# Optimization experiments

Hardware: AMD Instinct MI355X
Metric: run time of the kernel (lower is better)

Reference implementation:

```python
import jax, jax.numpy as jnp
import numpy as np

INIT_W = 0.1  # init_weight uniform range


def setup_inputs() -> dict:
    key = jax.random.key(0)
    kq, kk, kwq, kwk, ka = jax.random.split(key, 5)
    B, b, t_q, t_k = 2, 16, 64, 128
    qs = ks = nu = 512
    query = jax.random.normal(kq, (B, b, t_q, qs), dtype=jnp.float32)
    keys = jax.random.normal(kk, (B, b, t_k, ks), dtype=jnp.float32)
    # torch Linear weight layout: (out_features, in_features), per fusion slice
    Wq = (jax.random.uniform(kwq, (B, nu, qs), dtype=jnp.float32) * 2 - 1) * INIT_W
    Wk = (jax.random.uniform(kwk, (B, nu, ks), dtype=jnp.float32) * 2 - 1) * INIT_W
    linear_att = (jax.random.uniform(ka, (nu,), dtype=jnp.float32) * 2 - 1) * INIT_W
    return {"query": query, "keys": keys, "Wq": Wq, "Wk": Wk, "linear_att": linear_att}


def reference(query, keys, Wq, Wk, linear_att):
    # query: (B, b, t_q, query_size), keys: (B, b, t_k, key_size)
    # HFTA-fused linear projections (no bias): y = x @ W.T per fusion slice
    pq = jnp.einsum('Bbqi,Boi->Bbqo', query, Wq)   # (B, b, t_q, n)
    pk = jnp.einsum('Bbki,Boi->Bbko', keys, Wk)    # (B, b, t_k, n)
    # Bahdanau additive score: tanh(q + k) . v  (broadcast add over t_q x t_k)
    sum_qk = pq[:, :, :, None, :] + pk[:, :, None, :, :]   # (B, b, t_q, t_k, n)
    scores = jnp.einsum('Bbqkn,n->Bbqk', jnp.tanh(sum_qk), linear_att)
    scores_normalized = jax.nn.softmax(scores, axis=-1)    # (B, b, t_q, t_k)
    # context uses RAW keys (not projected)
    context = jnp.einsum('Bbqk,Bbkn->Bbqn', scores_normalized, keys)
    return context, scores_normalized
```

## Files before the change

### kernel.cpp

```cpp
#include <hip/hip_runtime.h>


#define DEV_INLINE __device__ __forceinline__

constexpr float C2    = 2.8853900817779268f;
constexpr float LOG2E = 1.4426950408889634f;

typedef _Float16 f16x8 __attribute__((ext_vector_type(8)));
typedef float    f32x16 __attribute__((ext_vector_type(16)));

DEV_INLINE unsigned int pk2(float a, float b) {
    auto h = __builtin_amdgcn_cvt_pkrtz(a, b);
    return __builtin_bit_cast(unsigned int, h);
}

#define GL2LDS16(g, l) __builtin_amdgcn_global_load_lds( \
    (const __attribute__((address_space(1))) void*)(g),  \
    (__attribute__((address_space(3))) void*)(l), 16, 0, 0)

__global__ __launch_bounds__(256)
void cvt_f16_kernel(const float* __restrict__ query, const float* __restrict__ keys,
                    const float* __restrict__ Wq,    const float* __restrict__ Wk,
                    uint2* __restrict__ dst)
{
    const int i4 = blockIdx.x * 256 + threadIdx.x;
    const float* src; int base;
    if (i4 < 262144)      { src = query; base = 0; }
    else if (i4 < 786432) { src = keys;  base = 262144; }
    else if (i4 < 917504) { src = Wq;    base = 786432; }
    else                  { src = Wk;    base = 917504; }
    const float4 v = *reinterpret_cast<const float4*>(src + (size_t)(i4 - base) * 4);
    dst[i4] = make_uint2(pk2(v.x, v.y), pk2(v.z, v.w));
}

__global__ __launch_bounds__(256)
void proj_mfma_kernel(const _Float16* __restrict__ X16,
                      float* __restrict__ pqT, float* __restrict__ pkT)
{
    __shared__ __align__(16) unsigned char smem[24576];

    const int bid = (blockIdx.x & 7) * 48 + (blockIdx.x >> 3);

    int Bi, mt, tt, tkshift;
    const _Float16 *Wb, *Xb; float* Y;
    if (bid < 128) {
        Bi = bid >> 6; mt = (bid >> 4) & 3; tt = bid & 15;
        Xb = X16 + ((size_t)Bi * 1024 + tt * 64) * 512;
        Wb = X16 + 3145728 + (size_t)Bi * 262144 + (size_t)(mt * 128) * 512;
        Y = pqT; tkshift = 6;
    } else {
        const int b2 = bid - 128;
        Bi = b2 >> 7; mt = (b2 >> 5) & 3; tt = b2 & 31;
        Xb = X16 + 1048576 + ((size_t)Bi * 2048 + tt * 64) * 512;
        Wb = X16 + 3670016 + (size_t)Bi * 262144 + (size_t)(mt * 128) * 512;
        Y = pkT; tkshift = 7;
    }
    const int tid = threadIdx.x;

    auto srcoff = [](int u) {
        const int row = u >> 2, s = (u & 3) ^ ((row >> 1) & 3);
        return (size_t)row * 512 + s * 8;
    };
    const _Float16* gA0 = Wb + srcoff(tid);
    const _Float16* gA1 = Wb + srcoff(tid + 256);
    const _Float16* gB  = Xb + srcoff(tid);
    unsigned char* const ldsA0 = smem + tid * 16;
    unsigned char* const ldsA1 = smem + 4096 + tid * 16;
    unsigned char* const ldsB  = smem + 8192 + tid * 16;

    const int wid = tid >> 6, lane = tid & 63;
    const int wm = wid >> 1, wn = wid & 1;
    const int r31 = lane & 31, h = lane >> 5;
    auto lofs = [](int row, int slot) {
        return row * 64 + ((slot ^ ((row >> 1) & 3)) * 16);
    };
    const int rowA0 = wm * 64 + r31, rowA1 = rowA0 + 32, rowB = wn * 32 + r31;
    const int a00 = lofs(rowA0, h),     a01 = lofs(rowA0, 2 + h);
    const int a10 = lofs(rowA1, h),     a11 = lofs(rowA1, 2 + h);
    const int b0  = 8192 + lofs(rowB, h), b1 = 8192 + lofs(rowB, 2 + h);

    f32x16 acc0, acc1;
#pragma unroll
    for (int i = 0; i < 16; ++i) { acc0[i] = 0.f; acc1[i] = 0.f; }

    GL2LDS16(gA0, ldsA0);
    GL2LDS16(gA1, ldsA1);
    GL2LDS16(gB,  ldsB);
    asm volatile("s_waitcnt vmcnt(0)" ::: "memory");
    __builtin_amdgcn_s_barrier();

    for (int ks = 0; ks < 16; ++ks) {
        const int buf = ks & 1;
        if (ks < 15) {
            const int ko = (ks + 1) * 32, bo = (buf ^ 1) * 12288;
            GL2LDS16(gA0 + ko, ldsA0 + bo);
            GL2LDS16(gA1 + ko, ldsA1 + bo);
            GL2LDS16(gB  + ko, ldsB  + bo);
        }
        const unsigned char* sb = smem + buf * 12288;
        const f16x8 fa00 = *reinterpret_cast<const f16x8*>(sb + a00);
        const f16x8 fa01 = *reinterpret_cast<const f16x8*>(sb + a01);
        const f16x8 fa10 = *reinterpret_cast<const f16x8*>(sb + a10);
        const f16x8 fa11 = *reinterpret_cast<const f16x8*>(sb + a11);
        const f16x8 fb0  = *reinterpret_cast<const f16x8*>(sb + b0);
        const f16x8 fb1  = *reinterpret_cast<const f16x8*>(sb + b1);
        acc0 = __builtin_amdgcn_mfma_f32_32x32x16_f16(fa00, fb0, acc0, 0, 0, 0);
        acc0 = __builtin_amdgcn_mfma_f32_32x32x16_f16(fa01, fb1, acc0, 0, 0, 0);
        acc1 = __builtin_amdgcn_mfma_f32_32x32x16_f16(fa10, fb0, acc1, 0, 0, 0);
        acc1 = __builtin_amdgcn_mfma_f32_32x32x16_f16(fa11, fb1, acc1, 0, 0, 0);
        if (ks < 15) {
            asm volatile("s_waitcnt vmcnt(0)" ::: "memory");
            __builtin_amdgcn_s_barrier();
        }
    }

    const int TK = 1 << tkshift;
    const int trow = tt * 64 + wn * 32 + r31;
    const int slice = Bi * 16 + (trow >> tkshift);
    const int t = trow & (TK - 1);
    const int nf0 = mt * 128 + wm * 64 + 4 * h;
#pragma unroll
    for (int ab = 0; ab < 2; ++ab) {
        const f32x16 acc = ab ? acc1 : acc0;
#pragma unroll
        for (int reg = 0; reg < 16; ++reg) {
            const int nf = nf0 + ab * 32 + (reg & 3) + 8 * (reg >> 2);
            Y[((size_t)(slice * 512 + nf) << tkshift) + t] = acc[reg] * C2;
        }
    }
}

DEV_INLINE float wave_rmax(float v) {
#pragma unroll
    for (int off = 32; off; off >>= 1) v = fmaxf(v, __shfl_xor(v, off, 64));
    return v;
}
DEV_INLINE float wave_rsum(float v) {
#pragma unroll
    for (int off = 32; off; off >>= 1) v += __shfl_xor(v, off, 64);
    return v;
}

__global__ __launch_bounds__(1024)
void score_ctx_kernel(const float* __restrict__ pqT,
                      const float* __restrict__ pkT,
                      const float* __restrict__ vatt,
                      const float* __restrict__ keys,
                      float* __restrict__ sc_out,
                      float* __restrict__ ctx)
{
    const int xcd = blockIdx.x & 7, ix = blockIdx.x >> 3;
    const int slice = xcd * 4 + (ix >> 4);
    const int q0    = (ix & 15) * 4;
    const int tid   = threadIdx.x;
    const int k     = tid & 127;
    const int nh    = tid >> 7;

    __shared__ __align__(16) float pql[512][4];
    __shared__ float wl[512];
    __shared__ float partial[7][4][128];
    __shared__ __align__(16) float sc[4][128];
    __shared__ __align__(16) float4 ctxp[4][128];
    __shared__ float wredm[8], wreds[8], wsum[8];

    if (tid < 512) {
        const float vv = vatt[tid];
        wl[tid] = -2.f * vv;
        const float4 q4 = *reinterpret_cast<const float4*>(
            pqT + ((size_t)slice * 512 + tid) * 64 + q0);
        *reinterpret_cast<float4*>(&pql[tid][0]) = q4;
        const float s = wave_rsum(vv);
        if ((tid & 63) == 0) wsum[tid >> 6] = s;
    }
    __syncthreads();
    float sumv = 0.f;
#pragma unroll
    for (int w = 0; w < 8; ++w) sumv += wsum[w];

    const float* __restrict__ pkp = pkT + ((size_t)slice * 512 + nh * 64) * 128 + k;
    float a0 = 0.f, a1 = 0.f, a2 = 0.f, a3 = 0.f;
#pragma unroll 4
    for (int n = 0; n < 64; ++n) {
        const float pk = pkp[(size_t)n * 128];
        const float4 pq4 = *reinterpret_cast<const float4*>(&pql[nh * 64 + n][0]);
        const float w = wl[nh * 64 + n];
        const float e0 = __builtin_amdgcn_exp2f(pq4.x + pk);
        const float e1 = __builtin_amdgcn_exp2f(pq4.y + pk);
        const float e2 = __builtin_amdgcn_exp2f(pq4.z + pk);
        const float e3 = __builtin_amdgcn_exp2f(pq4.w + pk);
        a0 = fmaf(w, __builtin_amdgcn_rcpf(e0 + 1.f), a0);
        a1 = fmaf(w, __builtin_amdgcn_rcpf(e1 + 1.f), a1);
        a2 = fmaf(w, __builtin_amdgcn_rcpf(e2 + 1.f), a2);
        a3 = fmaf(w, __builtin_amdgcn_rcpf(e3 + 1.f), a3);
    }
    if (nh) {
        partial[nh - 1][0][k] = a0; partial[nh - 1][1][k] = a1;
        partial[nh - 1][2][k] = a2; partial[nh - 1][3][k] = a3;
    }
    __syncthreads();
    if (!nh) {
        float s0 = a0 + sumv, s1 = a1 + sumv, s2 = a2 + sumv, s3 = a3 + sumv;
#pragma unroll
        for (int p = 0; p < 7; ++p) {
            s0 += partial[p][0][k]; s1 += partial[p][1][k];
            s2 += partial[p][2][k]; s3 += partial[p][3][k];
        }
        sc[0][k] = s0; sc[1][k] = s1; sc[2][k] = s2; sc[3][k] = s3;
    }
    __syncthreads();

    {
        const int j = nh & 3;
        float e = 0.f;
        if (tid < 512) {
            const float orig = sc[j][k];
            const float m0 = wave_rmax(orig);
            if ((tid & 63) == 0) wredm[tid >> 6] = m0;
            e = orig;
        }
        __syncthreads();
        if (tid < 512) {
            const float m = fmaxf(wredm[2 * j], wredm[2 * j + 1]);
            e = __builtin_amdgcn_exp2f((e - m) * LOG2E);
            const float ss = wave_rsum(e);
            if ((tid & 63) == 0) wreds[tid >> 6] = ss;
        }
        __syncthreads();
        if (tid < 512) {
            const float s = wreds[2 * j] + wreds[2 * j + 1];
            const float p = e * __builtin_amdgcn_rcpf(s);
            sc_out[((size_t)slice * 64 + q0 + j) * 128 + k] = p;
            sc[j][k] = p;
        }
    }
    __syncthreads();

    const int q = tid >> 8, n4 = k, ks = (tid >> 7) & 1;
    const float* __restrict__ kb = keys + (size_t)slice * 65536 + (size_t)ks * 64 * 512 + n4 * 4;
    float4 acc = {0.f, 0.f, 0.f, 0.f};
#pragma unroll 2
    for (int k4 = 0; k4 < 16; ++k4) {
        const float4 pv = *reinterpret_cast<const float4*>(&sc[q][ks * 64 + k4 * 4]);
        const float4 kv0 = *reinterpret_cast<const float4*>(kb + (size_t)(k4 * 4 + 0) * 512);
        const float4 kv1 = *reinterpret_cast<const float4*>(kb + (size_t)(k4 * 4 + 1) * 512);
        const float4 kv2 = *reinterpret_cast<const float4*>(kb + (size_t)(k4 * 4 + 2) * 512);
        const float4 kv3 = *reinterpret_cast<const float4*>(kb + (size_t)(k4 * 4 + 3) * 512);
        acc.x = fmaf(pv.x, kv0.x, acc.x); acc.y = fmaf(pv.x, kv0.y, acc.y);
        acc.z = fmaf(pv.x, kv0.z, acc.z); acc.w = fmaf(pv.x, kv0.w, acc.w);
        acc.x = fmaf(pv.y, kv1.x, acc.x); acc.y = fmaf(pv.y, kv1.y, acc.y);
        acc.z = fmaf(pv.y, kv1.z, acc.z); acc.w = fmaf(pv.y, kv1.w, acc.w);
        acc.x = fmaf(pv.z, kv2.x, acc.x); acc.y = fmaf(pv.z, kv2.y, acc.y);
        acc.z = fmaf(pv.z, kv2.z, acc.z); acc.w = fmaf(pv.z, kv2.w, acc.w);
        acc.x = fmaf(pv.w, kv3.x, acc.x); acc.y = fmaf(pv.w, kv3.y, acc.y);
        acc.z = fmaf(pv.w, kv3.z, acc.z); acc.w = fmaf(pv.w, kv3.w, acc.w);
    }
    if (ks) ctxp[q][n4] = acc;
    __syncthreads();
    if (!ks) {
        const float4 o = ctxp[q][n4];
        acc.x += o.x; acc.y += o.y; acc.z += o.z; acc.w += o.w;
        *reinterpret_cast<float4*>(ctx + ((size_t)slice * 64 + q0 + q) * 512 + n4 * 4) = acc;
    }
}

extern "C" void kernel_launch(void* const* d_in, const int* in_sizes, int n_in,
                              void* d_out, int out_size, void* d_ws, size_t ws_size,
                              hipStream_t stream)
{
    const float* query = (const float*)d_in[0];
    const float* keys  = (const float*)d_in[1];
    const float* Wq    = (const float*)d_in[2];
    const float* Wk    = (const float*)d_in[3];
    const float* vatt  = (const float*)d_in[4];

    float* ctx_out = (float*)d_out;
    float* sc_out  = ctx_out + (size_t)32 * 64 * 512;

    float* pqT = (float*)d_ws;
    float* pkT = pqT + (size_t)32 * 512 * 64;
    _Float16* X16 = (_Float16*)((char*)d_ws + 12 * 1024 * 1024);

    cvt_f16_kernel<<<dim3(4096), 256, 0, stream>>>(query, keys, Wq, Wk, (uint2*)X16);
    proj_mfma_kernel<<<dim3(384), 256, 0, stream>>>(X16, pqT, pkT);
    score_ctx_kernel<<<dim3(512), 1024, 0, stream>>>(pqT, pkT, vatt, keys, sc_out, ctx_out);
}
```

Measured before the change: 65.34 us.

## Reuse key loads across four queries in context GEMV and use bit-trick reciprocal

The context stage is restructured so each thread loads a key row once and applies it to all four queries, with the score buffer transposed to [k][q] for float4 reads. The reduction over eight key groups becomes a three-level shared-memory tree, which adds barriers. The score loop's hardware reciprocal is replaced by a bit-trick initial guess refined by two Newton iterations, presumably to move work off the transcendental unit at the cost of extra ALU ops and slightly different accuracy.

```diff
diff --git a/kernel.cpp b/kernel.cpp
--- a/kernel.cpp
+++ b/kernel.cpp
@@ -12,6 +12,13 @@
 DEV_INLINE unsigned int pk2(float a, float b) {
     auto h = __builtin_amdgcn_cvt_pkrtz(a, b);
     return __builtin_bit_cast(unsigned int, h);
+}
+
+DEV_INLINE float rcp_nr(float d) {
+    float y = __builtin_bit_cast(float, 0x7EF311C3u - __builtin_bit_cast(unsigned int, d));
+    y = y * (2.0f - d * y);
+    y = y * (2.0f - d * y);
+    return y;
 }
 
 #define GL2LDS16(g, l) __builtin_amdgcn_global_load_lds( \
@@ -159,8 +166,8 @@
     __shared__ __align__(16) float pql[512][4];
     __shared__ float wl[512];
     __shared__ float partial[7][4][128];
-    __shared__ __align__(16) float sc[4][128];
-    __shared__ __align__(16) float4 ctxp[4][128];
+    __shared__ __align__(16) float sc[128][4];
+    __shared__ __align__(16) float4 ctxp[4][4][128];
     __shared__ float wredm[8], wreds[8], wsum[8];
 
     if (tid < 512) {
@@ -188,10 +195,10 @@
         const float e1 = __builtin_amdgcn_exp2f(pq4.y + pk);
         const float e2 = __builtin_amdgcn_exp2f(pq4.z + pk);
         const float e3 = __builtin_amdgcn_exp2f(pq4.w + pk);
-        a0 = fmaf(w, __builtin_amdgcn_rcpf(e0 + 1.f), a0);
-        a1 = fmaf(w, __builtin_amdgcn_rcpf(e1 + 1.f), a1);
-        a2 = fmaf(w, __builtin_amdgcn_rcpf(e2 + 1.f), a2);
-        a3 = fmaf(w, __builtin_amdgcn_rcpf(e3 + 1.f), a3);
+        a0 = fmaf(w, rcp_nr(e0 + 1.f), a0);
+        a1 = fmaf(w, rcp_nr(e1 + 1.f), a1);
+        a2 = fmaf(w, rcp_nr(e2 + 1.f), a2);
+        a3 = fmaf(w, rcp_nr(e3 + 1.f), a3);
     }
     if (nh) {
         partial[nh - 1][0][k] = a0; partial[nh - 1][1][k] = a1;
@@ -205,7 +212,8 @@
             s0 += partial[p][0][k]; s1 += partial[p][1][k];
             s2 += partial[p][2][k]; s3 += partial[p][3][k];
         }
-        sc[0][k] = s0; sc[1][k] = s1; sc[2][k] = s2; sc[3][k] = s3;
+        float4 sv; sv.x = s0; sv.y = s1; sv.z = s2; sv.w = s3;
+        *reinterpret_cast<float4*>(&sc[k][0]) = sv;
     }
     __syncthreads();
 
@@ -213,7 +221,7 @@
         const int j = nh & 3;
         float e = 0.f;
         if (tid < 512) {
-            const float orig = sc[j][k];
+            const float orig = sc[k][j];
             const float m0 = wave_rmax(orig);
             if ((tid & 63) == 0) wredm[tid >> 6] = m0;
             e = orig;
@@ -230,36 +238,73 @@
             const float s = wreds[2 * j] + wreds[2 * j + 1];
             const float p = e * __builtin_amdgcn_rcpf(s);
             sc_out[((size_t)slice * 64 + q0 + j) * 128 + k] = p;
-            sc[j][k] = p;
-        }
-    }
-    __syncthreads();
-
-    const int q = tid >> 8, n4 = k, ks = (tid >> 7) & 1;
-    const float* __restrict__ kb = keys + (size_t)slice * 65536 + (size_t)ks * 64 * 512 + n4 * 4;
-    float4 acc = {0.f, 0.f, 0.f, 0.f};
-#pragma unroll 2
-    for (int k4 = 0; k4 < 16; ++k4) {
-        const float4 pv = *reinterpret_cast<const float4*>(&sc[q][ks * 64 + k4 * 4]);
-        const float4 kv0 = *reinterpret_cast<const float4*>(kb + (size_t)(k4 * 4 + 0) * 512);
-        const float4 kv1 = *reinterpret_cast<const float4*>(kb + (size_t)(k4 * 4 + 1) * 512);
-        const float4 kv2 = *reinterpret_cast<const float4*>(kb + (size_t)(k4 * 4 + 2) * 512);
-        const float4 kv3 = *reinterpret_cast<const float4*>(kb + (size_t)(k4 * 4 + 3) * 512);
-        acc.x = fmaf(pv.x, kv0.x, acc.x); acc.y = fmaf(pv.x, kv0.y, acc.y);
-        acc.z = fmaf(pv.x, kv0.z, acc.z); acc.w = fmaf(pv.x, kv0.w, acc.w);
-        acc.x = fmaf(pv.y, kv1.x, acc.x); acc.y = fmaf(pv.y, kv1.y, acc.y);
-        acc.z = fmaf(pv.y, kv1.z, acc.z); acc.w = fmaf(pv.y, kv1.w, acc.w);
-        acc.x = fmaf(pv.z, kv2.x, acc.x); acc.y = fmaf(pv.z, kv2.y, acc.y);
-        acc.z = fmaf(pv.z, kv2.z, acc.z); acc.w = fmaf(pv.z, kv2.w, acc.w);
-        acc.x = fmaf(pv.w, kv3.x, acc.x); acc.y = fmaf(pv.w, kv3.y, acc.y);
-        acc.z = fmaf(pv.w, kv3.z, acc.z); acc.w = fmaf(pv.w, kv3.w, acc.w);
-    }
-    if (ks) ctxp[q][n4] = acc;
-    __syncthreads();
-    if (!ks) {
-        const float4 o = ctxp[q][n4];
-        acc.x += o.x; acc.y += o.y; acc.z += o.z; acc.w += o.w;
-        *reinterpret_cast<float4*>(ctx + ((size_t)slice * 64 + q0 + q) * 512 + n4 * 4) = acc;
+            sc[k][j] = p;
+        }
+    }
+    __syncthreads();
+
+    const int kg = nh, n4 = k;
+    float4 acc0 = {0,0,0,0}, acc1 = {0,0,0,0}, acc2 = {0,0,0,0}, acc3 = {0,0,0,0};
+    const float* __restrict__ kb = keys + (size_t)slice * 65536 + (size_t)(kg * 16) * 512 + n4 * 4;
+#pragma unroll 4
+    for (int r = 0; r < 16; ++r) {
+        const float4 kv = *reinterpret_cast<const float4*>(kb + (size_t)r * 512);
+        const float4 pv = *reinterpret_cast<const float4*>(&sc[kg * 16 + r][0]);
+        acc0.x = fmaf(pv.x, kv.x, acc0.x); acc0.y = fmaf(pv.x, kv.y, acc0.y);
+        acc0.z = fmaf(pv.x, kv.z, acc0.z); acc0.w = fmaf(pv.x, kv.w, acc0.w);
+        acc1.x = fmaf(pv.y, kv.x, acc1.x); acc1.y = fmaf(pv.y, kv.y, acc1.y);
+        acc1.z = fmaf(pv.y, kv.z, acc1.z); acc1.w = fmaf(pv.y, kv.w, acc1.w);
+        acc2.x = fmaf(pv.z, kv.x, acc2.x); acc2.y = fmaf(pv.z, kv.y, acc2.y);
+        acc2.z = fmaf(pv.z, kv.z, acc2.z); acc2.w = fmaf(pv.z, kv.w, acc2.w);
+        acc3.x = fmaf(pv.w, kv.x, acc3.x); acc3.y = fmaf(pv.w, kv.y, acc3.y);
+        acc3.z = fmaf(pv.w, kv.z, acc3.z); acc3.w = fmaf(pv.w, kv.w, acc3.w);
+    }
+
+    if (kg >= 4) {
+        ctxp[kg - 4][0][n4] = acc0; ctxp[kg - 4][1][n4] = acc1;
+        ctxp[kg - 4][2][n4] = acc2; ctxp[kg - 4][3][n4] = acc3;
+    }
+    __syncthreads();
+    if (kg < 4) {
+        const float4 o0 = ctxp[kg][0][n4], o1 = ctxp[kg][1][n4];
+        const float4 o2 = ctxp[kg][2][n4], o3 = ctxp[kg][3][n4];
+        acc0.x += o0.x; acc0.y += o0.y; acc0.z += o0.z; acc0.w += o0.w;
+        acc1.x += o1.x; acc1.y += o1.y; acc1.z += o1.z; acc1.w += o1.w;
+        acc2.x += o2.x; acc2.y += o2.y; acc2.z += o2.z; acc2.w += o2.w;
+        acc3.x += o3.x; acc3.y += o3.y; acc3.z += o3.z; acc3.w += o3.w;
+    }
+    __syncthreads();
+    if (kg == 2 || kg == 3) {
+        ctxp[kg - 2][0][n4] = acc0; ctxp[kg - 2][1][n4] = acc1;
+        ctxp[kg - 2][2][n4] = acc2; ctxp[kg - 2][3][n4] = acc3;
+    }
+    __syncthreads();
+    if (kg < 2) {
+        const float4 o0 = ctxp[kg][0][n4], o1 = ctxp[kg][1][n4];
+        const float4 o2 = ctxp[kg][2][n4], o3 = ctxp[kg][3][n4];
+        acc0.x += o0.x; acc0.y += o0.y; acc0.z += o0.z; acc0.w += o0.w;
+        acc1.x += o1.x; acc1.y += o1.y; acc1.z += o1.z; acc1.w += o1.w;
+        acc2.x += o2.x; acc2.y += o2.y; acc2.z += o2.z; acc2.w += o2.w;
+        acc3.x += o3.x; acc3.y += o3.y; acc3.z += o3.z; acc3.w += o3.w;
+    }
+    __syncthreads();
+    if (kg == 1) {
+        ctxp[0][0][n4] = acc0; ctxp[0][1][n4] = acc1;
+        ctxp[0][2][n4] = acc2; ctxp[0][3][n4] = acc3;
+    }
+    __syncthreads();
+    if (kg == 0) {
+        const float4 o0 = ctxp[0][0][n4], o1 = ctxp[0][1][n4];
+        const float4 o2 = ctxp[0][2][n4], o3 = ctxp[0][3][n4];
+        acc0.x += o0.x; acc0.y += o0.y; acc0.z += o0.z; acc0.w += o0.w;
+        acc1.x += o1.x; acc1.y += o1.y; acc1.z += o1.z; acc1.w += o1.w;
+        acc2.x += o2.x; acc2.y += o2.y; acc2.z += o2.z; acc2.w += o2.w;
+        acc3.x += o3.x; acc3.y += o3.y; acc3.z += o3.z; acc3.w += o3.w;
+        float* cb = ctx + ((size_t)slice * 64 + q0) * 512 + n4 * 4;
+        *reinterpret_cast<float4*>(cb)             = acc0;
+        *reinterpret_cast<float4*>(cb + 512)       = acc1;
+        *reinterpret_cast<float4*>(cb + 2 * 512)   = acc2;
+        *reinterpret_cast<float4*>(cb + 3 * 512)   = acc3;
     }
 }
 
```

Result: faster. 62.72 us (-4.0%).
